# Kernel tuning notes

Measured on AMD Instinct MI355X. Metric: run time of the kernel, lower is better.

The kernel has to match this reference:

```python
import jax, jax.numpy as jnp
import numpy as np

B, N, DIM = 2, 512, 128
HEADS, DH = 4, 64
INNER = HEADS * DH            # 256
POS_HID = 64
MULT = 4                      # attn_mlp_hidden_mult
K = 16                        # num_neighbors


def setup_inputs() -> dict:
    key = jax.random.key(0)
    ks = jax.random.split(key, 10)
    w = lambda k, shape: jax.random.normal(k, shape, jnp.float32) * 0.02
    return {
        "x": jax.random.normal(ks[0], (B, N, DIM), jnp.float32),
        "pos": jax.random.normal(ks[1], (B, N, 3), jnp.float32),
        "mask": jnp.ones((B, N), dtype=bool),
        "w_qkv": w(ks[2], (DIM, 3 * INNER)),
        "w_out": w(ks[3], (INNER, DIM)),
        "b_out": jnp.zeros((DIM,), jnp.float32),
        "w_pos1": w(ks[4], (3, POS_HID)),
        "b_pos1": jnp.zeros((POS_HID,), jnp.float32),
        "w_pos2": w(ks[5], (POS_HID, INNER)),
        "b_pos2": jnp.zeros((INNER,), jnp.float32),
        # grouped 1x1 convs == per-head linear layers
        "w_attn1": w(ks[6], (HEADS, DH, MULT * DH)),
        "b_attn1": jnp.zeros((HEADS, MULT * DH), jnp.float32),
        "w_attn2": w(ks[7], (HEADS, MULT * DH, DH)),
        "b_attn2": jnp.zeros((HEADS, DH), jnp.float32),
    }


def reference(x, pos, mask, w_qkv, w_out, b_out, w_pos1, b_pos1, w_pos2, b_pos2,
              w_attn1, b_attn1, w_attn2, b_attn2):
    b, n, _ = x.shape
    h, d = HEADS, DH

    qkv = x @ w_qkv                                   # [b, n, 3*inner]
    q, k, v = jnp.split(qkv, 3, axis=-1)
    to_heads = lambda t: t.reshape(b, n, h, d).transpose(0, 2, 1, 3)  # b h n d
    q, k, v = map(to_heads, (q, k, v))

    # dense pairwise relative positions + pos MLP  [b, n, n, inner]
    rel_pos = pos[:, :, None, :] - pos[:, None, :, :]            # [b, n, n, 3]
    rpe = jax.nn.relu(rel_pos @ w_pos1 + b_pos1) @ w_pos2 + b_pos2

    # masked topk over pairwise distance (smallest K)
    rel_dist = jnp.linalg.norm(rel_pos, axis=-1)                 # [b, n, n]
    mask2 = mask[:, :, None] & mask[:, None, :]                  # [b, n, n]
    fmax = jnp.finfo(rel_dist.dtype).max
    rel_dist = jnp.where(mask2, rel_dist, fmax)
    _, idx = jax.lax.top_k(-rel_dist, K)                         # [b, n, K]

    # neighbor gathers (equivalent to torch batched_index_select over j)
    gather_hd = jax.vmap(lambda t, i: t[:, i, :])                # [h,n,d],[n,K] -> [h,n,K,d]
    k_nb = gather_hd(k, idx)                                     # [b, h, n, K, d]
    v_nb = gather_hd(v, idx)
    row = jnp.arange(n)[:, None]
    rpe_nb = jax.vmap(lambda r, i: r[row, i])(rpe, idx)          # [b, n, K, inner]
    rpe_nb = rpe_nb.reshape(b, n, K, h, d).transpose(0, 3, 1, 2, 4)  # [b,h,n,K,d]
    mask_nb = jax.vmap(lambda m, i: m[row, i])(mask2, idx)       # [b, n, K]

    # qk_rel gathered implicitly: (q_i - k_j)[j=idx] == q_i - k_nb
    attn_in = q[:, :, :, None, :] - k_nb + rpe_nb                # [b, h, n, K, d]

    # grouped 1x1 conv MLP == per-head MLP on last dim
    hid = jax.nn.relu(jnp.einsum('bhikd,hde->bhike', attn_in, w_attn1)
                      + b_attn1[None, :, None, None, :])
    sim = (jnp.einsum('bhike,hed->bhikd', hid, w_attn2)
           + b_attn2[None, :, None, None, :])                    # [b, h, n, K, d]

    sim = jnp.where(mask_nb[:, None, :, :, None], sim, -fmax)
    # torch: sim is [b, (h d), i, j]; softmax(dim=-2) is over i -> axis 2 here
    attn = jax.nn.softmax(sim, axis=2)

    v_full = v_nb + rpe_nb                                       # [b, h, n, K, d]
    agg = jnp.sum(attn * v_full, axis=3)                         # [b, h, n, d]
    agg = agg.transpose(0, 2, 1, 3).reshape(b, n, h * d)         # [b, n, inner]
    return agg @ w_out + b_out
```

## Files before the change

### kernel.cpp

```cpp
#include <hip/hip_runtime.h>

#define B_ 2
#define N_ 512
#define DIM_ 128
#define HEADS_ 4
#define DH_ 64
#define INNER_ 256
#define PH_ 64
#define HID2_ 256
#define KNB_ 16

typedef unsigned long long u64;
typedef unsigned int u32;
typedef unsigned short u16;
typedef __attribute__((ext_vector_type(8))) short bf16x8;
typedef __attribute__((ext_vector_type(8))) unsigned short us8;
typedef __attribute__((ext_vector_type(4))) float f32x4;

__device__ __forceinline__ float bf2f(u16 u) {
    union { float f; u32 u; } c; c.u = ((u32)u) << 16; return c.f;
}
__device__ __forceinline__ u16 f2bf(float f) {
    union { float f; u32 u; } c; c.f = f;
    u32 u = c.u;
    return (u16)((u + 0x7fffu + ((u >> 16) & 1u)) >> 16);
}
__device__ __forceinline__ u32 pack2(float lo, float hi) {
    return ((u32)f2bf(hi) << 16) | (u32)f2bf(lo);
}

__global__ __launch_bounds__(256) void k_front(
        const float* __restrict__ x, const float* __restrict__ pos, const float* __restrict__ w_qkv,
        const float* __restrict__ w_a1, const float* __restrict__ w_a2, const float* __restrict__ w_p2,
        u16* __restrict__ wf1, u16* __restrict__ wf2, u16* __restrict__ wfp,
        u16* __restrict__ qb, u16* __restrict__ kb, u16* __restrict__ vb,
        int* __restrict__ idx) {
    int blk = blockIdx.x;
    if (blk < 576) {
        int t = blk * 256 + threadIdx.x;
        if (t < 65536) {
            int jj = t & 7, lbig = (t >> 3) & 63, f = t >> 9;
            int s = f & 1, etL = (f >> 1) & 7, half = (f >> 4) & 1, h = f >> 5;
            int lr = lbig & 15, g = lbig >> 4;
            int d = s * 32 + g * 8 + jj, e = (half * 8 + etL) * 16 + lr;
            wf1[t] = f2bf(w_a1[((h * 64 + d) << 8) + e]);
        } else if (t < 131072) {
            int t2 = t - 65536;
            int jj = t2 & 7, lbig = (t2 >> 3) & 63, f = t2 >> 9;
            int s = f & 7, ct = (f >> 3) & 3, h = f >> 5;
            int lr = lbig & 15, g = lbig >> 4;
            int e = s * 32 + g * 8 + jj, c = ct * 16 + lr;
            wf2[t2] = f2bf(w_a2[(((h << 8) + e) << 6) + c]);
        } else {
            int t3 = t - 131072;
            int jj = t3 & 7, lbig = (t3 >> 3) & 63, f = t3 >> 9;
            int s = f & 1, ct = (f >> 1) & 3, h = f >> 3;
            int lr = lbig & 15, g = lbig >> 4;
            int e = s * 32 + g * 8 + jj, c = h * 64 + ct * 16 + lr;
            wfp[t3] = f2bf(w_p2[(e << 8) + c]);
        }
    } else if (blk < 704) {
        int bu = blk - 576;
        int b = bu >> 6;
        int n0 = (bu & 63) * 8;
        int t = threadIdx.x;
        __shared__ float xs[8][128];
        #pragma unroll
        for (int p = 0; p < 4; ++p) {
            int e = p * 256 + t;
            xs[e >> 7][e & 127] = x[((size_t)(b * N_ + n0) + (e >> 7)) * DIM_ + (e & 127)];
        }
        __syncthreads();
        float acc[3][8];
        #pragma unroll
        for (int cc = 0; cc < 3; ++cc)
            #pragma unroll
            for (int r = 0; r < 8; ++r) acc[cc][r] = 0.f;
        for (int c4 = 0; c4 < 32; ++c4) {
            float wv[3][4];
            #pragma unroll
            for (int dd = 0; dd < 4; ++dd)
                #pragma unroll
                for (int cc = 0; cc < 3; ++cc)
                    wv[cc][dd] = w_qkv[(size_t)(c4 * 4 + dd) * (3 * INNER_) + cc * INNER_ + t];
            #pragma unroll
            for (int r = 0; r < 8; ++r) {
                float4 xv = *(const float4*)&xs[r][c4 * 4];
                #pragma unroll
                for (int cc = 0; cc < 3; ++cc)
                    acc[cc][r] += xv.x * wv[cc][0] + xv.y * wv[cc][1] + xv.z * wv[cc][2] + xv.w * wv[cc][3];
            }
        }
        int h = t >> 6, d = t & 63;
        #pragma unroll
        for (int r = 0; r < 8; ++r) {
            size_t o = (((size_t)(b * HEADS_ + h)) * N_ + n0 + r) * DH_ + d;
            qb[o] = f2bf(acc[0][r]);
            kb[o] = f2bf(acc[1][r]);
            vb[o] = f2bf(acc[2][r]);
        }
    } else {
        int wave = (blk - 704) * 4 + (threadIdx.x >> 6);
        int lane = threadIdx.x & 63;
        int b = wave >> 9;
        float px = pos[(size_t)wave * 3 + 0];
        float py = pos[(size_t)wave * 3 + 1];
        float pz = pos[(size_t)wave * 3 + 2];
        u64 keys[8];
        #pragma unroll
        for (int s = 0; s < 8; ++s) {
            int j = s * 64 + lane;
            float dx = __fsub_rn(px, pos[(size_t)(b * N_ + j) * 3 + 0]);
            float dy = __fsub_rn(py, pos[(size_t)(b * N_ + j) * 3 + 1]);
            float dz = __fsub_rn(pz, pos[(size_t)(b * N_ + j) * 3 + 2]);
            float s2 = __fadd_rn(__fadd_rn(__fmul_rn(dx, dx), __fmul_rn(dy, dy)), __fmul_rn(dz, dz));
            float dist = __fsqrt_rn(s2);
            keys[s] = ((u64)__float_as_uint(dist) << 32) | (unsigned)j;
        }
        for (int r = 0; r < KNB_; ++r) {
            u64 m = keys[0];
            #pragma unroll
            for (int s = 1; s < 8; ++s) m = (keys[s] < m) ? keys[s] : m;
            #pragma unroll
            for (int off = 32; off >= 1; off >>= 1) {
                u64 o = __shfl_xor(m, off);
                m = (o < m) ? o : m;
            }
            if (lane == 0) idx[(size_t)wave * KNB_ + r] = (int)(m & 0xffffffffu);
            #pragma unroll
            for (int s = 0; s < 8; ++s) if (keys[s] == m) keys[s] = ~0ull;
        }
    }
}

__global__ __launch_bounds__(256, 2) void k_gather(
        const u16* __restrict__ qb, const u16* __restrict__ kb, const u16* __restrict__ vb,
        const int* __restrict__ idx, const float* __restrict__ pos,
        const float* __restrict__ w_p1, const float* __restrict__ b_p1,
        const float* __restrict__ b_p2, const u16* __restrict__ wfp,
        u16* __restrict__ ainb, u16* __restrict__ vf) {
    __shared__ u16 RP[4][2][16 * 72];
    __shared__ float PSM[1536];
    int t = threadIdx.x;
    int wv = t >> 6, l = t & 63, lr = l & 15, g = l >> 4;
    int blk = blockIdx.x;
    int b = blk >> 8;
    int i0 = (blk & 255) * 2;
    int h = wv, bh = b * HEADS_ + h;

    #pragma unroll
    for (int p = 0; p < 6; ++p)
        PSM[p * 256 + t] = pos[(size_t)b * 1536 + p * 256 + t];

    int jn[2];
    us8 qv[2][2], kv[2][2], vvb[2][2];
    #pragma unroll
    for (int ii = 0; ii < 2; ++ii) {
        int i = i0 + ii, bi = (b << 9) + i;
        int j = idx[(bi << 4) + lr];
        jn[ii] = j;
        #pragma unroll
        for (int s = 0; s < 2; ++s) {
            qv[ii][s]  = *(const us8*)&qb[(size_t)(bh * N_ + i) * 64 + s * 32 + g * 8];
            kv[ii][s]  = *(const us8*)&kb[(size_t)(bh * N_ + j) * 64 + s * 32 + g * 8];
            vvb[ii][s] = *(const us8*)&vb[(size_t)(bh * N_ + j) * 64 + s * 32 + g * 8];
        }
    }
    __syncthreads();

    bf16x8 hidp[2][2];
    #pragma unroll
    for (int ii = 0; ii < 2; ++ii) {
        int i = i0 + ii, j = jn[ii];
        float rx = PSM[i * 3 + 0] - PSM[j * 3 + 0];
        float ry = PSM[i * 3 + 1] - PSM[j * 3 + 1];
        float rz = PSM[i * 3 + 2] - PSM[j * 3 + 2];
        #pragma unroll
        for (int s = 0; s < 2; ++s) {
            u16 tmp[8];
            #pragma unroll
            for (int jj = 0; jj < 8; ++jj) {
                int e = s * 32 + g * 8 + jj;
                float hh = b_p1[e] + rx * w_p1[e] + ry * w_p1[PH_ + e] + rz * w_p1[2 * PH_ + e];
                tmp[jj] = f2bf(fmaxf(hh, 0.f));
            }
            hidp[ii][s] = *(bf16x8*)tmp;
        }
    }

    {
        bf16x8 Ar[4][2];
        #pragma unroll
        for (int ct = 0; ct < 4; ++ct)
            #pragma unroll
            for (int s = 0; s < 2; ++s)
                Ar[ct][s] = *(const bf16x8*)&wfp[(size_t)((((h << 2) + ct) << 1) + s) * 512 + l * 8];
        #pragma unroll
        for (int ct = 0; ct < 4; ++ct) {
            f32x4 C0 = {0.f, 0.f, 0.f, 0.f}, C1 = {0.f, 0.f, 0.f, 0.f};
            #pragma unroll
            for (int s = 0; s < 2; ++s) {
                C0 = __builtin_amdgcn_mfma_f32_16x16x32_bf16(Ar[ct][s], hidp[0][s], C0, 0, 0, 0);
                C1 = __builtin_amdgcn_mfma_f32_16x16x32_bf16(Ar[ct][s], hidp[1][s], C1, 0, 0, 0);
            }
            float4 bias = *(const float4*)&b_p2[h * 64 + ct * 16 + g * 4];
            uint2 o0, o1;
            o0.x = pack2(C0[0] + bias.x, C0[1] + bias.y);
            o0.y = pack2(C0[2] + bias.z, C0[3] + bias.w);
            o1.x = pack2(C1[0] + bias.x, C1[1] + bias.y);
            o1.y = pack2(C1[2] + bias.z, C1[3] + bias.w);
            *(uint2*)&RP[wv][0][lr * 72 + ct * 16 + g * 4] = o0;
            *(uint2*)&RP[wv][1][lr * 72 + ct * 16 + g * 4] = o1;
        }
    }

    #pragma unroll
    for (int ii = 0; ii < 2; ++ii) {
        int i = i0 + ii;
        #pragma unroll
        for (int s = 0; s < 2; ++s) {
            bf16x8 rp = *(const bf16x8*)&RP[wv][ii][lr * 72 + s * 32 + g * 8];
            us8 rpu = *(const us8*)&rp;
            u16 ta[8], tv[8];
            #pragma unroll
            for (int jj = 0; jj < 8; ++jj) {
                float rpf = bf2f(rpu[jj]);
                ta[jj] = f2bf(bf2f(qv[ii][s][jj]) - bf2f(kv[ii][s][jj]) + rpf);
                tv[jj] = f2bf(bf2f(vvb[ii][s][jj]) + rpf);
            }
            *(bf16x8*)&ainb[((size_t)((bh * N_ + i) * 2 + s)) * 512 + l * 8] = *(bf16x8*)ta;
            *(bf16x8*)&vf[(size_t)(((bh * N_ + i) << 4) + lr) * 64 + s * 32 + g * 8] = *(bf16x8*)tv;
        }
    }
}

__global__ __launch_bounds__(256) void k_mlp(
        const u16* __restrict__ ainb,
        const u16* __restrict__ wf1, const u16* __restrict__ wf2,
        const float* __restrict__ b_a1, const float* __restrict__ b_a2,
        u16* __restrict__ sim) {
    __shared__ u16 W1[16384];
    __shared__ u16 W2[16384];
    __shared__ u16 HID[4][2][16 * 136];
    int t = threadIdx.x;
    int wv = t >> 6, l = t & 63, lr = l & 15, g = l >> 4;
    int blk = blockIdx.x;
    int bh = blk >> 6;
    int h = bh & 3;
    int i0 = (blk & 63) * 8 + wv * 2;

    bf16x8 ain[2][2];
    #pragma unroll
    for (int ii = 0; ii < 2; ++ii) {
        int i = i0 + ii;
        #pragma unroll
        for (int s = 0; s < 2; ++s)
            ain[ii][s] = *(const bf16x8*)&ainb[((size_t)((bh * N_ + i) * 2 + s)) * 512 + l * 8];
    }

    {
        const u16* s1 = wf1 + ((size_t)h << 14);
        const u16* s2 = wf2 + ((size_t)h << 14);
        #pragma unroll
        for (int p = 0; p < 8; ++p) {
            int e = p * 2048 + t * 8;
            *(bf16x8*)&W1[e] = *(const bf16x8*)&s1[e];
            *(bf16x8*)&W2[e] = *(const bf16x8*)&s2[e];
        }
    }
    __syncthreads();

    f32x4 C2[2][4];
    #pragma unroll
    for (int ii = 0; ii < 2; ++ii)
        #pragma unroll
        for (int ct = 0; ct < 4; ++ct) C2[ii][ct] = (f32x4){0.f, 0.f, 0.f, 0.f};
    #pragma unroll
    for (int half = 0; half < 2; ++half) {
        #pragma unroll
        for (int etL = 0; etL < 8; ++etL) {
            int et = half * 8 + etL;
            f32x4 C0 = {0.f, 0.f, 0.f, 0.f}, C1 = {0.f, 0.f, 0.f, 0.f};
            #pragma unroll
            for (int s = 0; s < 2; ++s) {
                bf16x8 A = *(const bf16x8*)&W1[((((half << 3) + etL) << 1) + s) * 512 + l * 8];
                C0 = __builtin_amdgcn_mfma_f32_16x16x32_bf16(A, ain[0][s], C0, 0, 0, 0);
                C1 = __builtin_amdgcn_mfma_f32_16x16x32_bf16(A, ain[1][s], C1, 0, 0, 0);
            }
            float4 bias = *(const float4*)&b_a1[h * 256 + et * 16 + g * 4];
            uint2 p0, p1;
            p0.x = pack2(fmaxf(C0[0] + bias.x, 0.f), fmaxf(C0[1] + bias.y, 0.f));
            p0.y = pack2(fmaxf(C0[2] + bias.z, 0.f), fmaxf(C0[3] + bias.w, 0.f));
            p1.x = pack2(fmaxf(C1[0] + bias.x, 0.f), fmaxf(C1[1] + bias.y, 0.f));
            p1.y = pack2(fmaxf(C1[2] + bias.z, 0.f), fmaxf(C1[3] + bias.w, 0.f));
            *(uint2*)&HID[wv][0][lr * 136 + etL * 16 + g * 4] = p0;
            *(uint2*)&HID[wv][1][lr * 136 + etL * 16 + g * 4] = p1;
        }
        #pragma unroll
        for (int sL = 0; sL < 4; ++sL) {
            int s = half * 4 + sL;
            bf16x8 B0 = *(const bf16x8*)&HID[wv][0][lr * 136 + sL * 32 + g * 8];
            bf16x8 B1 = *(const bf16x8*)&HID[wv][1][lr * 136 + sL * 32 + g * 8];
            #pragma unroll
            for (int ct = 0; ct < 4; ++ct) {
                bf16x8 A = *(const bf16x8*)&W2[((ct << 3) + s) * 512 + l * 8];
                C2[0][ct] = __builtin_amdgcn_mfma_f32_16x16x32_bf16(A, B0, C2[0][ct], 0, 0, 0);
                C2[1][ct] = __builtin_amdgcn_mfma_f32_16x16x32_bf16(A, B1, C2[1][ct], 0, 0, 0);
            }
        }
    }
    #pragma unroll
    for (int ii = 0; ii < 2; ++ii) {
        int i = i0 + ii;
        #pragma unroll
        for (int ct = 0; ct < 4; ++ct) {
            float4 bias = *(const float4*)&b_a2[h * 64 + ct * 16 + g * 4];
            uint2 o;
            o.x = pack2(C2[ii][ct][0] + bias.x, C2[ii][ct][1] + bias.y);
            o.y = pack2(C2[ii][ct][2] + bias.z, C2[ii][ct][3] + bias.w);
            *(uint2*)&sim[(size_t)(((bh * N_ + i) << 4) + lr) * 64 + ct * 16 + g * 4] = o;
        }
    }
}

__global__ __launch_bounds__(256) void k_stats(const u16* __restrict__ sim, float* __restrict__ P) {
    int blk = blockIdx.x;
    int half = blk & 1, ks = (blk >> 1) & 15, bh = blk >> 5;
    int d0 = (threadIdx.x & 15) * 4;
    int nc = threadIdx.x >> 4;
    __shared__ float red[16][69];
    size_t base = ((size_t)(bh * N_ + half * 256 + nc * 16) * 16 + ks) * 64 + d0;
    float s0 = 0.f, s1 = 0.f, s2 = 0.f, s3 = 0.f;
    #pragma unroll
    for (int nn = 0; nn < 16; ++nn) {
        uint2 u = *(const uint2*)&sim[base + (size_t)nn * 1024];
        s0 += __expf(bf2f((u16)(u.x & 0xffff)));
        s1 += __expf(bf2f((u16)(u.x >> 16)));
        s2 += __expf(bf2f((u16)(u.y & 0xffff)));
        s3 += __expf(bf2f((u16)(u.y >> 16)));
    }
    red[nc][d0 + 0] = s0; red[nc][d0 + 1] = s1;
    red[nc][d0 + 2] = s2; red[nc][d0 + 3] = s3;
    __syncthreads();
    int t = threadIdx.x;
    if (t < 64) {
        float s = 0.f;
        #pragma unroll
        for (int c = 0; c < 16; ++c) s += red[c][t];
        P[(size_t)blk * 64 + t] = s;
    }
}

__global__ __launch_bounds__(256) void k_agg_out(
        const u16* __restrict__ sim, const u16* __restrict__ vf, const float* __restrict__ P,
        const float* __restrict__ w, const float* __restrict__ bo, float* __restrict__ out) {
    int blk = blockIdx.x;
    int b = blk >> 8;
    int i0 = (blk & 255) * 2;
    int t = threadIdx.x;
    __shared__ float ag[2][260];
    {
        int h = t >> 6, d = t & 63;
        int bh = b * HEADS_ + h;
        float Rk[16];
        #pragma unroll
        for (int ks = 0; ks < 16; ++ks) {
            int pbase = ((bh << 5) + (ks << 1)) * 64 + d;
            Rk[ks] = 1.f / (P[pbase] + P[pbase + 64]);
        }
        #pragma unroll
        for (int r = 0; r < 2; ++r) {
            size_t base = (size_t)((bh * N_ + i0 + r) << 4) * 64 + d;
            float acc = 0.f;
            #pragma unroll
            for (int ks = 0; ks < 16; ++ks) {
                float p = __expf(bf2f(sim[base + (size_t)ks * 64])) * Rk[ks];
                acc += p * bf2f(vf[base + (size_t)ks * 64]);
            }
            ag[r][h * 64 + d] = acc;
        }
    }
    __syncthreads();
    int c = t & 127, rg = t >> 7;
    float acc = bo[c];
    for (int k4 = 0; k4 < 64; ++k4) {
        float4 a4 = *(const float4*)&ag[rg][k4 * 4];
        acc += a4.x * w[(size_t)(k4 * 4 + 0) * DIM_ + c] + a4.y * w[(size_t)(k4 * 4 + 1) * DIM_ + c]
             + a4.z * w[(size_t)(k4 * 4 + 2) * DIM_ + c] + a4.w * w[(size_t)(k4 * 4 + 3) * DIM_ + c];
    }
    out[(size_t)((b << 9) + i0 + rg) * DIM_ + c] = acc;
}

extern "C" void kernel_launch(void* const* d_in, const int* in_sizes, int n_in,
                              void* d_out, int out_size, void* d_ws, size_t ws_size,
                              hipStream_t stream) {
    const float* x      = (const float*)d_in[0];
    const float* pos    = (const float*)d_in[1];
    const float* w_qkv  = (const float*)d_in[3];
    const float* w_out  = (const float*)d_in[4];
    const float* b_out  = (const float*)d_in[5];
    const float* w_pos1 = (const float*)d_in[6];
    const float* b_pos1 = (const float*)d_in[7];
    const float* w_pos2 = (const float*)d_in[8];
    const float* b_pos2 = (const float*)d_in[9];
    const float* w_a1   = (const float*)d_in[10];
    const float* b_a1   = (const float*)d_in[11];
    const float* w_a2   = (const float*)d_in[12];
    const float* b_a2   = (const float*)d_in[13];
    float* out = (float*)d_out;

    char* W = (char*)d_ws;
    u16*  qb   = (u16*)W;            W += 524288;
    u16*  kb   = (u16*)W;            W += 524288;
    u16*  vb   = (u16*)W;            W += 524288;
    int*  idx  = (int*)W;            W += 65536;
    u16*  sim  = (u16*)W;            W += 8388608;
    u16*  vf   = (u16*)W;            W += 8388608;
    u16*  ainb = (u16*)W;            W += 8388608;
    float* P   = (float*)W;          W += 65536;
    u16*  wf1  = (u16*)W;            W += 131072;
    u16*  wf2  = (u16*)W;            W += 131072;
    u16*  wfp  = (u16*)W;            W += 32768;

    k_front<<<960, 256, 0, stream>>>(x, pos, w_qkv, w_a1, w_a2, w_pos2,
                                     wf1, wf2, wfp, qb, kb, vb, idx);
    k_gather<<<512, 256, 0, stream>>>(qb, kb, vb, idx, pos, w_pos1, b_pos1, b_pos2, wfp,
                                      ainb, vf);
    k_mlp<<<512, 256, 0, stream>>>(ainb, wf1, wf2, b_a1, b_a2, sim);
    k_stats<<<256, 256, 0, stream>>>(sim, P);
    k_agg_out<<<512, 256, 0, stream>>>(sim, vf, P, w_out, b_out, out);
}
```

Measured before the change: 59.52 us.

## Fuse softmax column-sum stats into MLP kernel and stream weights from global

The separate k_stats kernel is removed. k_mlp now accumulates exp(sim) per (bh, k, d) column, reduces it across its four waves in shared memory, and atomically adds the partial into P, which is zeroed by a memset at the start. The MLP weights are no longer staged into LDS; each wave loads its MFMA A-operands directly from global/L2 into registers, with launch_bounds raised to allow two blocks per CU. This saves one launch and a full re-read of sim, and cuts LDS use. In exchange it adds float atomics whose summation order is nondeterministic and repeats weight loads across waves.

```diff
diff --git a/kernel.cpp b/kernel.cpp
--- a/kernel.cpp
+++ b/kernel.cpp
@@ -234,14 +234,13 @@
     }
 }
 
-__global__ __launch_bounds__(256) void k_mlp(
+__global__ __launch_bounds__(256, 2) void k_mlp(
         const u16* __restrict__ ainb,
         const u16* __restrict__ wf1, const u16* __restrict__ wf2,
         const float* __restrict__ b_a1, const float* __restrict__ b_a2,
-        u16* __restrict__ sim) {
-    __shared__ u16 W1[16384];
-    __shared__ u16 W2[16384];
+        u16* __restrict__ sim, float* __restrict__ P) {
     __shared__ u16 HID[4][2][16 * 136];
+    __shared__ float PL[4][16][64];
     int t = threadIdx.x;
     int wv = t >> 6, l = t & 63, lr = l & 15, g = l >> 4;
     int blk = blockIdx.x;
@@ -258,18 +257,6 @@
             ain[ii][s] = *(const bf16x8*)&ainb[((size_t)((bh * N_ + i) * 2 + s)) * 512 + l * 8];
     }
 
-    {
-        const u16* s1 = wf1 + ((size_t)h << 14);
-        const u16* s2 = wf2 + ((size_t)h << 14);
-        #pragma unroll
-        for (int p = 0; p < 8; ++p) {
-            int e = p * 2048 + t * 8;
-            *(bf16x8*)&W1[e] = *(const bf16x8*)&s1[e];
-            *(bf16x8*)&W2[e] = *(const bf16x8*)&s2[e];
-        }
-    }
-    __syncthreads();
-
     f32x4 C2[2][4];
     #pragma unroll
     for (int ii = 0; ii < 2; ++ii)
@@ -277,15 +264,20 @@
         for (int ct = 0; ct < 4; ++ct) C2[ii][ct] = (f32x4){0.f, 0.f, 0.f, 0.f};
     #pragma unroll
     for (int half = 0; half < 2; ++half) {
+        bf16x8 A1[8][2];
+        #pragma unroll
+        for (int etL = 0; etL < 8; ++etL)
+            #pragma unroll
+            for (int s = 0; s < 2; ++s)
+                A1[etL][s] = *(const bf16x8*)&wf1[(size_t)(((((h << 1) + half) << 3) + etL) * 2 + s) * 512 + l * 8];
         #pragma unroll
         for (int etL = 0; etL < 8; ++etL) {
             int et = half * 8 + etL;
             f32x4 C0 = {0.f, 0.f, 0.f, 0.f}, C1 = {0.f, 0.f, 0.f, 0.f};
             #pragma unroll
             for (int s = 0; s < 2; ++s) {
-                bf16x8 A = *(const bf16x8*)&W1[((((half << 3) + etL) << 1) + s) * 512 + l * 8];
-                C0 = __builtin_amdgcn_mfma_f32_16x16x32_bf16(A, ain[0][s], C0, 0, 0, 0);
-                C1 = __builtin_amdgcn_mfma_f32_16x16x32_bf16(A, ain[1][s], C1, 0, 0, 0);
+                C0 = __builtin_amdgcn_mfma_f32_16x16x32_bf16(A1[etL][s], ain[0][s], C0, 0, 0, 0);
+                C1 = __builtin_amdgcn_mfma_f32_16x16x32_bf16(A1[etL][s], ain[1][s], C1, 0, 0, 0);
             }
             float4 bias = *(const float4*)&b_a1[h * 256 + et * 16 + g * 4];
             uint2 p0, p1;
@@ -297,57 +289,67 @@
             *(uint2*)&HID[wv][1][lr * 136 + etL * 16 + g * 4] = p1;
         }
         #pragma unroll
-        for (int sL = 0; sL < 4; ++sL) {
-            int s = half * 4 + sL;
-            bf16x8 B0 = *(const bf16x8*)&HID[wv][0][lr * 136 + sL * 32 + g * 8];
-            bf16x8 B1 = *(const bf16x8*)&HID[wv][1][lr * 136 + sL * 32 + g * 8];
-            #pragma unroll
-            for (int ct = 0; ct < 4; ++ct) {
-                bf16x8 A = *(const bf16x8*)&W2[((ct << 3) + s) * 512 + l * 8];
-                C2[0][ct] = __builtin_amdgcn_mfma_f32_16x16x32_bf16(A, B0, C2[0][ct], 0, 0, 0);
-                C2[1][ct] = __builtin_amdgcn_mfma_f32_16x16x32_bf16(A, B1, C2[1][ct], 0, 0, 0);
-            }
-        }
-    }
+        for (int chunk = 0; chunk < 2; ++chunk) {
+            bf16x8 A2[4][2];
+            #pragma unroll
+            for (int ct = 0; ct < 4; ++ct)
+                #pragma unroll
+                for (int ss = 0; ss < 2; ++ss) {
+                    int s = half * 4 + chunk * 2 + ss;
+                    A2[ct][ss] = *(const bf16x8*)&wf2[(size_t)((((h << 2) + ct) << 3) + s) * 512 + l * 8];
+                }
+            #pragma unroll
+            for (int ss = 0; ss < 2; ++ss) {
+                int sL = chunk * 2 + ss;
+                bf16x8 B0 = *(const bf16x8*)&HID[wv][0][lr * 136 + sL * 32 + g * 8];
+                bf16x8 B1 = *(const bf16x8*)&HID[wv][1][lr * 136 + sL * 32 + g * 8];
+                #pragma unroll
+                for (int ct = 0; ct < 4; ++ct) {
+                    C2[0][ct] = __builtin_amdgcn_mfma_f32_16x16x32_bf16(A2[ct][ss], B0, C2[0][ct], 0, 0, 0);
+                    C2[1][ct] = __builtin_amdgcn_mfma_f32_16x16x32_bf16(A2[ct][ss], B1, C2[1][ct], 0, 0, 0);
+                }
+            }
+        }
+    }
+    float ps[4][4];
+    #pragma unroll
+    for (int ct = 0; ct < 4; ++ct)
+        #pragma unroll
+        for (int q = 0; q < 4; ++q) ps[ct][q] = 0.f;
     #pragma unroll
     for (int ii = 0; ii < 2; ++ii) {
         int i = i0 + ii;
         #pragma unroll
         for (int ct = 0; ct < 4; ++ct) {
             float4 bias = *(const float4*)&b_a2[h * 64 + ct * 16 + g * 4];
+            u16 v0 = f2bf(C2[ii][ct][0] + bias.x);
+            u16 v1 = f2bf(C2[ii][ct][1] + bias.y);
+            u16 v2 = f2bf(C2[ii][ct][2] + bias.z);
+            u16 v3 = f2bf(C2[ii][ct][3] + bias.w);
             uint2 o;
-            o.x = pack2(C2[ii][ct][0] + bias.x, C2[ii][ct][1] + bias.y);
-            o.y = pack2(C2[ii][ct][2] + bias.z, C2[ii][ct][3] + bias.w);
+            o.x = ((u32)v1 << 16) | v0;
+            o.y = ((u32)v3 << 16) | v2;
             *(uint2*)&sim[(size_t)(((bh * N_ + i) << 4) + lr) * 64 + ct * 16 + g * 4] = o;
-        }
-    }
-}
-
-__global__ __launch_bounds__(256) void k_stats(const u16* __restrict__ sim, float* __restrict__ P) {
-    int blk = blockIdx.x;
-    int half = blk & 1, ks = (blk >> 1) & 15, bh = blk >> 5;
-    int d0 = (threadIdx.x & 15) * 4;
-    int nc = threadIdx.x >> 4;
-    __shared__ float red[16][69];
-    size_t base = ((size_t)(bh * N_ + half * 256 + nc * 16) * 16 + ks) * 64 + d0;
-    float s0 = 0.f, s1 = 0.f, s2 = 0.f, s3 = 0.f;
-    #pragma unroll
-    for (int nn = 0; nn < 16; ++nn) {
-        uint2 u = *(const uint2*)&sim[base + (size_t)nn * 1024];
-        s0 += __expf(bf2f((u16)(u.x & 0xffff)));
-        s1 += __expf(bf2f((u16)(u.x >> 16)));
-        s2 += __expf(bf2f((u16)(u.y & 0xffff)));
-        s3 += __expf(bf2f((u16)(u.y >> 16)));
-    }
-    red[nc][d0 + 0] = s0; red[nc][d0 + 1] = s1;
-    red[nc][d0 + 2] = s2; red[nc][d0 + 3] = s3;
+            ps[ct][0] += __expf(bf2f(v0));
+            ps[ct][1] += __expf(bf2f(v1));
+            ps[ct][2] += __expf(bf2f(v2));
+            ps[ct][3] += __expf(bf2f(v3));
+        }
+    }
+    #pragma unroll
+    for (int ct = 0; ct < 4; ++ct)
+        #pragma unroll
+        for (int q = 0; q < 4; ++q)
+            PL[wv][lr][ct * 16 + g * 4 + q] = ps[ct][q];
     __syncthreads();
-    int t = threadIdx.x;
-    if (t < 64) {
-        float s = 0.f;
-        #pragma unroll
-        for (int c = 0; c < 16; ++c) s += red[c][t];
-        P[(size_t)blk * 64 + t] = s;
+    {
+        #pragma unroll
+        for (int q2 = 0; q2 < 4; ++q2) {
+            int e = t * 4 + q2;
+            int ks = e >> 6, d = e & 63;
+            float s4 = PL[0][ks][d] + PL[1][ks][d] + PL[2][ks][d] + PL[3][ks][d];
+            atomicAdd(&P[(bh << 10) + e], s4);
+        }
     }
 }
 
@@ -364,10 +366,8 @@
         int bh = b * HEADS_ + h;
         float Rk[16];
         #pragma unroll
-        for (int ks = 0; ks < 16; ++ks) {
-            int pbase = ((bh << 5) + (ks << 1)) * 64 + d;
-            Rk[ks] = 1.f / (P[pbase] + P[pbase + 64]);
-        }
+        for (int ks = 0; ks < 16; ++ks)
+            Rk[ks] = 1.f / P[(bh << 10) + (ks << 6) + d];
         #pragma unroll
         for (int r = 0; r < 2; ++r) {
             size_t base = (size_t)((bh * N_ + i0 + r) << 4) * 64 + d;
@@ -417,16 +417,16 @@
     u16*  sim  = (u16*)W;            W += 8388608;
     u16*  vf   = (u16*)W;            W += 8388608;
     u16*  ainb = (u16*)W;            W += 8388608;
-    float* P   = (float*)W;          W += 65536;
+    float* P   = (float*)W;          W += 32768;
     u16*  wf1  = (u16*)W;            W += 131072;
     u16*  wf2  = (u16*)W;            W += 131072;
     u16*  wfp  = (u16*)W;            W += 32768;
 
+    hipMemsetAsync(P, 0, 32768, stream);
     k_front<<<960, 256, 0, stream>>>(x, pos, w_qkv, w_a1, w_a2, w_pos2,
                                      wf1, wf2, wfp, qb, kb, vb, idx);
     k_gather<<<512, 256, 0, stream>>>(qb, kb, vb, idx, pos, w_pos1, b_pos1, b_pos2, wfp,
                                       ainb, vf);
-    k_mlp<<<512, 256, 0, stream>>>(ainb, wf1, wf2, b_a1, b_a2, sim);
-    k_stats<<<256, 256, 0, stream>>>(sim, P);
+    k_mlp<<<512, 256, 0, stream>>>(ainb, wf1, wf2, b_a1, b_a2, sim, P);
     k_agg_out<<<512, 256, 0, stream>>>(sim, vf, P, w_out, b_out, out);
 }
```

After: 66.88 us. 12.3% more time.
